# Optimization experiments

Hardware: AMD Instinct MI355X
Metric: run time of the kernel (lower is better)

Reference implementation:

```python
import jax, jax.numpy as jnp
import numpy as np

B, S = 64, 256
F, H, V = 512, 2048, 32000
PAD = 0
LN_EPS = 1e-5


def setup_inputs() -> dict:
    key = jax.random.key(0)
    ks = jax.random.split(key, 10)
    inputs = jax.random.randint(ks[0], (B, S), 0, V, dtype=jnp.int64)
    targets = jax.random.randint(ks[1], (B, S), 0, V, dtype=jnp.int64)
    # parameters (kaiming-ish / torch-default-ish scales)
    see = jax.random.normal(ks[2], (2 * F, F), jnp.float32) * (2.0 / (2 * F)) ** 0.5
    bias = jnp.zeros((F,), jnp.float32)
    W_in = jax.random.normal(ks[3], (H, F), jnp.float32) * (1.0 / F) ** 0.5
    b_in = jnp.zeros((H,), jnp.float32)
    W_out = jax.random.normal(ks[4], (F, H), jnp.float32) * (1.0 / H) ** 0.5
    b_out = jnp.zeros((F,), jnp.float32)
    ln_g = jnp.ones((F,), jnp.float32)
    ln_b = jnp.zeros((F,), jnp.float32)
    emb = jax.random.normal(ks[5], (V, F), jnp.float32)
    return {"inputs": inputs, "targets": targets, "see": see, "bias": bias,
            "W_in": W_in, "b_in": b_in, "W_out": W_out, "b_out": b_out,
            "ln_g": ln_g, "ln_b": ln_b, "emb": emb}


def _layernorm(x, g, b):
    mu = jnp.mean(x, axis=-1, keepdims=True)
    var = jnp.mean((x - mu) ** 2, axis=-1, keepdims=True)
    return (x - mu) * jax.lax.rsqrt(var + LN_EPS) * g + b


def reference(inputs, targets, see, bias, W_in, b_in, W_out, b_out, ln_g, ln_b, emb):
    emb_m = emb.at[PAD].set(0.0)  # padding_idx row is zero
    inv_sqrt_f = 1.0 / (F ** 0.5)

    def step(state, xy):
        idx, tgt = xy                      # [B], [B]
        vecs = emb_m[idx]                  # [B,F]
        gate = jax.nn.sigmoid(jnp.concatenate([vecs, state], axis=-1) @ see + bias)
        cont = state * gate + vecs * (1.0 - gate)
        h = jax.nn.relu(_layernorm(cont, ln_g, ln_b) @ W_in.T + b_in)
        out = h @ W_out.T + b_out          # [B,F]
        logits = (out @ emb_m.T) * inv_sqrt_f  # [B,V]
        logp = jax.nn.log_softmax(logits, axis=-1)
        nll = -jnp.take_along_axis(logp, tgt[:, None], axis=1)[:, 0]
        mask = (tgt != PAD).astype(logits.dtype)
        li = jnp.sum(nll * mask) / jnp.maximum(jnp.sum(mask), 1.0)
        return cont, li

    xs = (inputs.T, targets.T)  # [S,B]
    _, losses = jax.lax.scan(step, jnp.zeros((inputs.shape[0], F), emb.dtype), xs)
    return jnp.mean(losses)
```

## Files before the change

### kernel.cpp

```cpp
#include <hip/hip_runtime.h>
#include <hip/hip_fp8.h>

#define F_DIM 512
#define H_DIM 2048
#define V_DIM 32000
#define B_DIM 64
#define S_DIM 256
#define ROWS (S_DIM*B_DIM)
#define NT_LOG 250
#define SCALE 0.04419417382415922f
#define LSE_OFF 40.0f

typedef __attribute__((ext_vector_type(8))) short  short8;
typedef __attribute__((ext_vector_type(4))) float  floatx4;

static __device__ inline unsigned short f2bf(float x){
  unsigned int u = __float_as_uint(x);
  u += 0x7fffu + ((u >> 16) & 1u);
  return (unsigned short)(u >> 16);
}
static __device__ inline float bf2f(unsigned short u){
  return __uint_as_float(((unsigned int)u) << 16);
}
static __device__ inline unsigned char f2fp8(float x){
  __hip_fp8_e4m3 q(x);
  return q.__x;
}
static __device__ inline int sw8(int row, int col){
  int g = (col >> 3) & 7;
  int chunk = ((g >> 1) ^ ((row >> 1) & 3));
  int lob = (g & 1) ^ ((row >> 3) & 1);
  return (col & ~63) | (chunk << 4) | (lob << 3) | (col & 7);
}
static __device__ inline float wsum(float v){
  #pragma unroll
  for(int m = 32; m > 0; m >>= 1) v += __shfl_xor(v, m);
  return v;
}
static __device__ inline void load_lds16(const void* g, void* l){
  __builtin_amdgcn_global_load_lds((const __attribute__((address_space(1))) void*)g,
                                   (__attribute__((address_space(3))) void*)l, 16, 0, 0);
}

__global__ __launch_bounds__(256) void cast_w(const float* __restrict__ src,
                                              unsigned short* __restrict__ dst, int n){
  int i = blockIdx.x*256 + threadIdx.x;
  int stride = gridDim.x*256;
  for(; i < n; i += stride) dst[i] = f2bf(src[i]);
}
__global__ __launch_bounds__(256) void cast_emb(const float* __restrict__ src,
    unsigned short* __restrict__ dst, unsigned char* __restrict__ d8){
  int i = blockIdx.x*256 + threadIdx.x;
  int stride = gridDim.x*256;
  for(; i < V_DIM*F_DIM; i += stride){
    float v = (i < F_DIM) ? 0.f : src[i];
    dst[i] = f2bf(v);
    int row = i >> 9, col = i & 511;
    d8[(long)row*512 + sw8(row, col)] = f2fp8(v);
  }
}

__global__ __launch_bounds__(256) void prep_see(const float* __restrict__ see,
    unsigned short* __restrict__ TT, unsigned char* __restrict__ B8){
  int n = blockIdx.x;
  for(int k = threadIdx.x; k < 512; k += 256){
    TT[n*512 + k] = f2bf(see[(long)k*512 + n]);
    B8[n*512 + k] = f2fp8(see[(long)(512+k)*512 + n]);
  }
}

__global__ __launch_bounds__(256) void gather_vecs(const float* __restrict__ emb,
    const int* __restrict__ inp, unsigned short* __restrict__ V){
  long row = (long)blockIdx.x*4 + (threadIdx.x >> 6);
  int l = threadIdx.x & 63;
  int t = (int)(row >> 6), b = (int)(row & 63);
  int idx = inp[b*S_DIM + t];
  short8 o;
  if (idx == 0){
    #pragma unroll
    for(int i=0;i<8;i++) o[i] = 0;
  } else {
    const float* e = emb + (long)idx*F_DIM + l*8;
    float4 a = *(const float4*)e;
    float4 bq = *(const float4*)(e + 4);
    o[0]=(short)f2bf(a.x); o[1]=(short)f2bf(a.y); o[2]=(short)f2bf(a.z); o[3]=(short)f2bf(a.w);
    o[4]=(short)f2bf(bq.x);o[5]=(short)f2bf(bq.y);o[6]=(short)f2bf(bq.z);o[7]=(short)f2bf(bq.w);
  }
  *(short8*)(V + row*F_DIM + l*8) = o;
}

__global__ __launch_bounds__(512, 1) void recurrence_batch(
    const unsigned int* __restrict__ ZV,
    const unsigned char* __restrict__ W8,
    unsigned short* __restrict__ CONTB)
{
  __shared__ unsigned char stt[2][16][520];

  const int tid = threadIdx.x;
  const int w  = tid >> 6;
  const int l  = tid & 63;
  const int rl = l & 15, rq = l >> 4;
  const int wg = blockIdx.x;
  const int colb = w*64;

  long Bfr[16][4];
  #pragma unroll
  for(int c=0;c<16;c++)
    #pragma unroll
    for(int tl=0;tl<4;tl++)
      Bfr[c][tl] = *(const long*)(W8 + (long)(colb + tl*16 + rl)*512 + c*32 + rq*8);

  float s_old[16];
  #pragma unroll
  for(int i=0;i<16;i++) s_old[i] = 0.f;

  const unsigned int* zbase = ZV + (long)(wg*16 + rq*4)*512 + colb + rl;
  unsigned short* cbase = CONTB + ((long)wg*16 + rq*4)*512 + colb + rl;

  unsigned int zv[16];
  #pragma unroll
  for(int tl=0;tl<4;tl++)
    #pragma unroll
    for(int r=0;r<4;r++)
      zv[tl*4+r] = zbase[(long)r*512 + tl*16];

  for(int t = 0; t < S_DIM; t++){
    unsigned int zvn[16];
    if (t+1 < S_DIM){
      const unsigned int* zp = zbase + (long)(t+1)*64*512;
      #pragma unroll
      for(int tl=0;tl<4;tl++)
        #pragma unroll
        for(int r=0;r<4;r++)
          zvn[tl*4+r] = zp[(long)r*512 + tl*16];
    }

    asm volatile("s_waitcnt lgkmcnt(0)" ::: "memory");
    __builtin_amdgcn_s_barrier();
    asm volatile("" ::: "memory");

    floatx4 acc[4];
    #pragma unroll
    for(int tl=0;tl<4;tl++) acc[tl] = (floatx4)0.f;

    if (t > 0){
      const unsigned char* sb = &stt[(t-1)&1][0][0];
      #pragma unroll
      for(int c=0;c<16;c++){
        long a = *(const long*)(sb + rl*520 + c*32 + rq*8);
        #pragma unroll
        for(int tl=0;tl<4;tl++)
          acc[tl] = __builtin_amdgcn_mfma_f32_16x16x32_fp8_fp8(a, Bfr[c][tl], acc[tl], 0, 0, 0);
      }
    }

    unsigned short* cw = cbase + (long)t*64*512;
    unsigned char* swb = &stt[t&1][0][0] + rq*4*520 + colb + rl;
    #pragma unroll
    for(int tl=0;tl<4;tl++){
      float sv[4];
      #pragma unroll
      for(int r=0;r<4;r++){
        unsigned int p = zv[tl*4+r];
        float z = __uint_as_float(p << 16) + acc[tl][r];
        float v = __uint_as_float(p & 0xffff0000u);
        float e = __expf(-z);
        float g = __builtin_amdgcn_rcpf(1.f + e);
        float s = fmaf(s_old[tl*4+r] - v, g, v);
        s_old[tl*4+r] = s;
        sv[r] = s;
      }
      #pragma unroll
      for(int pr=0; pr<2; pr++){
        unsigned int bfp, f8p;
        asm("v_cvt_pk_bf16_f32 %0, %1, %2" : "=v"(bfp) : "v"(sv[pr*2]), "v"(sv[pr*2+1]));
        asm("v_cvt_pk_fp8_f32 %0, %1, %2"  : "=v"(f8p) : "v"(sv[pr*2]), "v"(sv[pr*2+1]));
        cw[(long)(pr*2)*512   + tl*16] = (unsigned short)(bfp & 0xffffu);
        cw[(long)(pr*2+1)*512 + tl*16] = (unsigned short)(bfp >> 16);
        swb[(pr*2)*520   + tl*16] = (unsigned char)(f8p & 0xffu);
        swb[(pr*2+1)*520 + tl*16] = (unsigned char)((f8p >> 8) & 0xffu);
      }
    }

    if (t+1 < S_DIM){
      #pragma unroll
      for(int i=0;i<16;i++) zv[i] = zvn[i];
    }
  }
}

__global__ __launch_bounds__(256) void ln_kernel(const unsigned short* __restrict__ contb,
    const float* __restrict__ lg, const float* __restrict__ lb,
    unsigned short* __restrict__ xln)
{
  const int wid = threadIdx.x >> 6, l = threadIdx.x & 63;
  const long row = (long)blockIdx.x*4 + wid;
  short8 xv = *(const short8*)(contb + row*F_DIM + l*8);
  float v[8];
  #pragma unroll
  for(int i=0;i<8;i++) v[i] = bf2f((unsigned short)xv[i]);
  float s = 0.f;
  #pragma unroll
  for(int i=0;i<8;i++) s += v[i];
  s = wsum(s);
  float mu = s * (1.f/512.f);
  float q = 0.f;
  #pragma unroll
  for(int i=0;i<8;i++){ float d = v[i]-mu; q += d*d; }
  q = wsum(q);
  float rs = rsqrtf(q*(1.f/512.f) + 1e-5f);
  short8 o;
  #pragma unroll
  for(int i=0;i<8;i++)
    o[i] = (short)f2bf((v[i]-mu)*rs*lg[l*8+i] + lb[l*8+i]);
  *(short8*)(xln + row*F_DIM + l*8) = o;
}

template<int MODE>
__global__ __launch_bounds__(256) void gemm_bt(
    const unsigned short* __restrict__ A,
    const unsigned short* __restrict__ Bm,
    const float* __restrict__ bias,
    unsigned short* __restrict__ C,
    unsigned char* __restrict__ C8,
    const unsigned short* __restrict__ Vsrc,
    unsigned int* __restrict__ ZVout,
    int M, int N, int K, int tiles_m, int tiles_n)
{
  __shared__ short As[128*64];
  __shared__ short Bs[128*64];

  const int bid = blockIdx.x;
  const int mt = bid % tiles_m;
  const int nt = bid / tiles_m;
  const long m0 = (long)mt * 128;
  const long n0 = (long)nt * 128;
  const int tid = threadIdx.x;
  const int l = tid & 63;
  const int wid = tid >> 6;
  const int wr = wid >> 1, wc = wid & 1;
  const int rl = l & 15, rq = l >> 4;

  const short* Ag = (const short*)A + m0 * K;
  const short* Bg = (const short*)Bm + n0 * K;
  const int grow = tid >> 3;
  const int kp = tid & 7;
  const int ksw = (kp ^ (grow & 7)) * 8;

  floatx4 acc[4][4];
  #pragma unroll
  for(int i=0;i<4;i++)
    #pragma unroll
    for(int j=0;j<4;j++) acc[i][j] = (floatx4)0.f;

  for(int k0 = 0; k0 < K; k0 += 64){
    __syncthreads();
    #pragma unroll
    for(int ro = 0; ro < 128; ro += 32){
      load_lds16(Ag + (long)(ro + grow)*K + k0 + ksw, (void*)(As + (ro+grow)*64 + kp*8));
      load_lds16(Bg + (long)(ro + grow)*K + k0 + ksw, (void*)(Bs + (ro+grow)*64 + kp*8));
    }
    __syncthreads();
    #pragma unroll
    for(int kb = 0; kb < 64; kb += 32){
      const int cb = kb >> 3;
      const int cl = ((cb + rq) ^ (rl & 7)) * 8;
      short8 af[4], bfr[4];
      #pragma unroll
      for(int i=0;i<4;i++) af[i]  = *(const short8*)(As + (wr*64 + i*16 + rl)*64 + cl);
      #pragma unroll
      for(int j=0;j<4;j++) bfr[j] = *(const short8*)(Bs + (wc*64 + j*16 + rl)*64 + cl);
      #pragma unroll
      for(int i=0;i<4;i++)
        #pragma unroll
        for(int j=0;j<4;j++)
          acc[i][j] = __builtin_amdgcn_mfma_f32_16x16x32_bf16(af[i], bfr[j], acc[i][j], 0, 0, 0);
    }
  }

  const long mb = m0 + wr*64;
  const long nb = n0 + wc*64;
  #pragma unroll
  for(int j=0;j<4;j++){
    float bj = bias[nb + j*16 + rl];
    #pragma unroll
    for(int i=0;i<4;i++){
      #pragma unroll
      for(int r=0;r<4;r++){
        float v = acc[i][j][r] + bj;
        if (MODE == 0) v = fmaxf(v, 0.f);
        int rowI = (int)(mb + i*16 + rq*4 + r);
        int colI = (int)(nb + j*16 + rl);
        long idx = (long)rowI*N + colI;
        if (MODE == 5){
          ZVout[idx] = ((unsigned)Vsrc[idx] << 16) | (unsigned)f2bf(v);
        } else {
          C[idx] = f2bf(v);
          if (MODE == 4) C8[(long)rowI*512 + sw8(rowI, colI)] = f2fp8(v);
        }
      }
    }
  }
}

__global__ __launch_bounds__(256) void gemm_f8_logits(
    const unsigned char* __restrict__ A8,
    const unsigned char* __restrict__ B8,
    float* __restrict__ part,
    int M, int N, int K, int tiles_m, int tiles_n)
{
  __shared__ unsigned char As8[2][128*64];
  __shared__ unsigned char Bs8[2][128*64];
  __shared__ float sm2[2][64][2];

  const int bid = blockIdx.x;
  const int mt = bid % tiles_m;
  const int nt = bid / tiles_m;
  const long m0 = (long)mt * 128;
  const long n0 = (long)nt * 128;
  const int tid = threadIdx.x;
  const int l = tid & 63;
  const int wid = tid >> 6;
  const int wr = wid >> 1, wc = wid & 1;
  const int rl = l & 15, rq = l >> 4;

  const unsigned char* Ag = A8 + m0 * K;
  const unsigned char* Bg = B8 + n0 * K;
  const int grow = tid >> 2;
  const int kp = tid & 3;

  floatx4 acc[4][4];
  #pragma unroll
  for(int i=0;i<4;i++)
    #pragma unroll
    for(int j=0;j<4;j++) acc[i][j] = (floatx4)0.f;

  const int rsw = (rl >> 1) & 3;
  const int rhi = (rl >> 3) & 1;

  const int nkt = K >> 6;

  #define STAGE_F8(bb, kk) do {                                               \
    const long kof = (long)(kk)*64 + kp*16;                                   \
    load_lds16(Ag + (long)grow*K       + kof, (void*)(&As8[bb][grow*64       + kp*16])); \
    load_lds16(Ag + (long)(64+grow)*K  + kof, (void*)(&As8[bb][(64+grow)*64  + kp*16])); \
    load_lds16(Bg + (long)grow*K       + kof, (void*)(&Bs8[bb][grow*64       + kp*16])); \
    load_lds16(Bg + (long)(64+grow)*K  + kof, (void*)(&Bs8[bb][(64+grow)*64  + kp*16])); \
  } while(0)

  STAGE_F8(0, 0);
  STAGE_F8(1, 1);

  for(int t = 0; t < nkt; t++){
    if (t < nkt-1) asm volatile("s_waitcnt vmcnt(4)" ::: "memory");
    else           asm volatile("s_waitcnt vmcnt(0)" ::: "memory");
    __builtin_amdgcn_s_barrier();
    __builtin_amdgcn_sched_barrier(0);

    const unsigned char* Abuf = &As8[t & 1][0];
    const unsigned char* Bbuf = &Bs8[t & 1][0];
    long af[2][4], bfr[2][4];
    #pragma unroll
    for(int kb = 0; kb < 2; kb++){
      const int g = (kb << 2) + rq;
      const int cl = ((((g >> 1) ^ rsw)) << 4) | ((((g & 1) ^ rhi)) << 3);
      #pragma unroll
      for(int i=0;i<4;i++) af[kb][i]  = *(const long*)(Abuf + (wr*64 + i*16 + rl)*64 + cl);
      #pragma unroll
      for(int j=0;j<4;j++) bfr[kb][j] = *(const long*)(Bbuf + (wc*64 + j*16 + rl)*64 + cl);
    }
    asm volatile("s_waitcnt lgkmcnt(0)" ::: "memory");
    __builtin_amdgcn_sched_barrier(0);
    __builtin_amdgcn_s_barrier();
    __builtin_amdgcn_sched_barrier(0);

    if (t+2 < nkt) STAGE_F8(t & 1, t+2);

    __builtin_amdgcn_s_setprio(1);
    #pragma unroll
    for(int kb = 0; kb < 2; kb++)
      #pragma unroll
      for(int i=0;i<4;i++)
        #pragma unroll
        for(int j=0;j<4;j++)
          acc[i][j] = __builtin_amdgcn_mfma_f32_16x16x32_fp8_fp8(af[kb][i], bfr[kb][j], acc[i][j], 0, 0, 0);
    __builtin_amdgcn_s_setprio(0);
  }
  #undef STAGE_F8

  #pragma unroll
  for(int i=0;i<4;i++){
    #pragma unroll
    for(int r=0;r<4;r++){
      float sv = 0.f;
      #pragma unroll
      for(int j=0;j<4;j++) sv += __expf(acc[i][j][r]*SCALE - LSE_OFF);
      #pragma unroll
      for(int d=1; d<16; d<<=1) sv += __shfl_xor(sv, d);
      if (rl == 0) sm2[wr][i*16 + rq*4 + r][wc] = sv;
    }
  }
  __syncthreads();
  if (tid < 128){
    int wr2 = tid >> 6, rowl = tid & 63;
    part[(m0 + wr2*64 + rowl)*tiles_n + nt] = sm2[wr2][rowl][0] + sm2[wr2][rowl][1];
  }
}

__global__ __launch_bounds__(256) void tlogit_kernel(const unsigned short* __restrict__ outb,
    const unsigned short* __restrict__ embb, const int* __restrict__ tgt,
    float* __restrict__ TL)
{
  long gw = (long)blockIdx.x*4 + (threadIdx.x >> 6);
  int l = threadIdx.x & 63;
  int t = (int)(gw >> 6), b = (int)(gw & 63);
  int tg = tgt[b*S_DIM + t];
  const unsigned short* o = outb + gw*F_DIM;
  const unsigned short* e = embb + (long)tg*F_DIM;
  short8 ov = *(const short8*)(o + l*8);
  short8 ev = *(const short8*)(e + l*8);
  float s = 0.f;
  #pragma unroll
  for(int i=0;i<8;i++) s += bf2f((unsigned short)ov[i]) * bf2f((unsigned short)ev[i]);
  s = wsum(s);
  if (l == 0) TL[gw] = s * SCALE;
}

__global__ __launch_bounds__(256) void lse_kernel(const float* __restrict__ part,
    const float* __restrict__ TL, float* __restrict__ nll)
{
  long row = (long)blockIdx.x*4 + (threadIdx.x >> 6);
  int l = threadIdx.x & 63;
  float S = 0.f;
  for(int c = l; c < NT_LOG; c += 64)
    S += part[row*NT_LOG + c];
  S = wsum(S);
  if (l == 0) nll[row] = (LSE_OFF + logf(S)) - TL[row];
}

__global__ __launch_bounds__(256) void loss_kernel(const float* __restrict__ nll,
    const int* __restrict__ tgt, float* __restrict__ out)
{
  int t = threadIdx.x;
  float s = 0.f; int cnt = 0;
  for(int b = 0; b < B_DIM; b++){
    int v = tgt[b*S_DIM + t];
    if (v != 0){ s += nll[(long)t*B_DIM + b]; cnt++; }
  }
  float li = s / fmaxf((float)cnt, 1.f);
  li = wsum(li);
  __shared__ float red[4];
  if ((t & 63) == 0) red[t >> 6] = li;
  __syncthreads();
  if (t == 0) out[0] = (red[0]+red[1]+red[2]+red[3]) * (1.f/256.f);
}

extern "C" void kernel_launch(void* const* d_in, const int* in_sizes, int n_in,
                              void* d_out, int out_size, void* d_ws, size_t ws_size,
                              hipStream_t stream)
{
  const int*   inp   = (const int*)d_in[0];
  const int*   tgt   = (const int*)d_in[1];
  const float* see   = (const float*)d_in[2];
  const float* bias  = (const float*)d_in[3];
  const float* W_in  = (const float*)d_in[4];
  const float* b_in  = (const float*)d_in[5];
  const float* W_out = (const float*)d_in[6];
  const float* b_out = (const float*)d_in[7];
  const float* ln_g  = (const float*)d_in[8];
  const float* ln_b  = (const float*)d_in[9];
  const float* emb   = (const float*)d_in[10];

  char* p = (char*)d_ws;
  unsigned short* CONTB= (unsigned short*)p; p += (size_t)ROWS*F_DIM*2;
  unsigned short* Hb   = (unsigned short*)p; p += (size_t)ROWS*H_DIM*2;
  unsigned short* OUTb = (unsigned short*)p; p += (size_t)ROWS*F_DIM*2;
  unsigned short* EMBb = (unsigned short*)p; p += (size_t)V_DIM*F_DIM*2;
  unsigned char* EMB8  = (unsigned char*)p;  p += (size_t)V_DIM*F_DIM;
  unsigned short* WINb = (unsigned short*)p; p += (size_t)H_DIM*F_DIM*2;
  unsigned short* WOUTb= (unsigned short*)p; p += (size_t)F_DIM*H_DIM*2;
  float* TL            = (float*)p;          p += (size_t)ROWS*4;
  float* NLL           = (float*)p;          p += (size_t)ROWS*4;
  unsigned short* VECSb= (unsigned short*)p; p += (size_t)ROWS*F_DIM*2;
  unsigned int* ZV     = (unsigned int*)p;   p += (size_t)ROWS*F_DIM*4;
  unsigned short* SEETT= (unsigned short*)p; p += (size_t)F_DIM*F_DIM*2;
  unsigned char* SEEB8 = (unsigned char*)p;  p += (size_t)F_DIM*F_DIM;
  unsigned short* XLN  = (unsigned short*)ZV;
  unsigned char* OUT8  = (unsigned char*)VECSb;
  float* PART          = (float*)Hb;

  cast_emb<<<4096, 256, 0, stream>>>(emb, EMBb, EMB8);
  cast_w<<<2048, 256, 0, stream>>>(W_in,  WINb,  H_DIM*F_DIM);
  cast_w<<<2048, 256, 0, stream>>>(W_out, WOUTb, F_DIM*H_DIM);
  prep_see<<<512, 256, 0, stream>>>(see, SEETT, SEEB8);
  gather_vecs<<<ROWS/4, 256, 0, stream>>>(emb, inp, VECSb);

  gemm_bt<5><<<128*4, 256, 0, stream>>>(VECSb, SEETT, bias, nullptr, nullptr,
                                        VECSb, ZV, ROWS, F_DIM, F_DIM, 128, 4);

  recurrence_batch<<<4, 512, 0, stream>>>(ZV, SEEB8, CONTB);

  ln_kernel<<<ROWS/4, 256, 0, stream>>>(CONTB, ln_g, ln_b, XLN);
  gemm_bt<0><<<128*16, 256, 0, stream>>>(XLN,  WINb,  b_in,  Hb,   nullptr,
                                         nullptr, nullptr, ROWS, H_DIM, F_DIM, 128, 16);
  gemm_bt<4><<<128*4,  256, 0, stream>>>(Hb,   WOUTb, b_out, OUTb, OUT8,
                                         nullptr, nullptr, ROWS, F_DIM, H_DIM, 128, 4);
  tlogit_kernel<<<ROWS/4, 256, 0, stream>>>(OUTb, EMBb, tgt, TL);
  gemm_f8_logits<<<128*NT_LOG, 256, 0, stream>>>(OUT8, EMB8, PART, ROWS, V_DIM, F_DIM, 128, NT_LOG);
  lse_kernel<<<ROWS/4, 256, 0, stream>>>(PART, TL, NLL);
  loss_kernel<<<1, 256, 0, stream>>>(NLL, tgt, (float*)d_out);
}
```

Baseline: 1.269 ms.

## Use 16x16x128 scaled FP8 MFMA and vectorized permuted ZV loads in recurrence

The serial recurrence kernel replaces 16 K-steps of 16x16x32 fp8 MFMA with 4 K-steps of the gfx950 16x16x128 scaled f8f6f4 MFMA, using unit scales. The A fragments now come from LDS as 32-byte reads, with the row pitch padded from 520 to 560. The ZV producer GEMM writes columns in a permuted order so each thread can read its 16 z/v values as four 128-bit loads. The next-step ZV prefetch moves to the end of the loop. The goal is fewer MFMA issues and fewer load instructions on the latency-bound sequential critical path. The risk is that the later prefetch exposes global-load latency.

```diff
diff --git a/kernel.cpp b/kernel.cpp
--- a/kernel.cpp
+++ b/kernel.cpp
@@ -13,6 +13,9 @@
 
 typedef __attribute__((ext_vector_type(8))) short  short8;
 typedef __attribute__((ext_vector_type(4))) float  floatx4;
+typedef __attribute__((ext_vector_type(4))) int    intx4;
+typedef __attribute__((ext_vector_type(8))) int    i32x8;
+typedef __attribute__((ext_vector_type(4))) unsigned int uix4;
 
 static __device__ inline unsigned short f2bf(float x){
   unsigned int u = __float_as_uint(x);
@@ -31,6 +34,9 @@
   int chunk = ((g >> 1) ^ ((row >> 1) & 3));
   int lob = (g & 1) ^ ((row >> 3) & 1);
   return (col & ~63) | (chunk << 4) | (lob << 3) | (col & 7);
+}
+static __device__ inline int zvperm(int c){
+  return (c & ~63) | ((c & 15) << 2) | ((c >> 4) & 3);
 }
 static __device__ inline float wsum(float v){
   #pragma unroll
@@ -94,7 +100,7 @@
     const unsigned char* __restrict__ W8,
     unsigned short* __restrict__ CONTB)
 {
-  __shared__ unsigned char stt[2][16][520];
+  __shared__ unsigned char stt[2][16][560];
 
   const int tid = threadIdx.x;
   const int w  = tid >> 6;
@@ -103,38 +109,25 @@
   const int wg = blockIdx.x;
   const int colb = w*64;
 
-  long Bfr[16][4];
-  #pragma unroll
-  for(int c=0;c<16;c++)
+  i32x8 Bfr[4][4];
+  #pragma unroll
+  for(int kt=0;kt<4;kt++)
     #pragma unroll
     for(int tl=0;tl<4;tl++)
-      Bfr[c][tl] = *(const long*)(W8 + (long)(colb + tl*16 + rl)*512 + c*32 + rq*8);
+      Bfr[kt][tl] = *(const i32x8*)(W8 + (long)(colb + tl*16 + rl)*512 + kt*128 + rq*32);
 
   float s_old[16];
   #pragma unroll
   for(int i=0;i<16;i++) s_old[i] = 0.f;
 
-  const unsigned int* zbase = ZV + (long)(wg*16 + rq*4)*512 + colb + rl;
+  const unsigned int* zbase = ZV + (long)(wg*16 + rq*4)*512 + colb + rl*4;
   unsigned short* cbase = CONTB + ((long)wg*16 + rq*4)*512 + colb + rl;
 
-  unsigned int zv[16];
-  #pragma unroll
-  for(int tl=0;tl<4;tl++)
-    #pragma unroll
-    for(int r=0;r<4;r++)
-      zv[tl*4+r] = zbase[(long)r*512 + tl*16];
+  uix4 zv[4];
+  #pragma unroll
+  for(int r=0;r<4;r++) zv[r] = *(const uix4*)(zbase + (long)r*512);
 
   for(int t = 0; t < S_DIM; t++){
-    unsigned int zvn[16];
-    if (t+1 < S_DIM){
-      const unsigned int* zp = zbase + (long)(t+1)*64*512;
-      #pragma unroll
-      for(int tl=0;tl<4;tl++)
-        #pragma unroll
-        for(int r=0;r<4;r++)
-          zvn[tl*4+r] = zp[(long)r*512 + tl*16];
-    }
-
     asm volatile("s_waitcnt lgkmcnt(0)" ::: "memory");
     __builtin_amdgcn_s_barrier();
     asm volatile("" ::: "memory");
@@ -143,25 +136,35 @@
     #pragma unroll
     for(int tl=0;tl<4;tl++) acc[tl] = (floatx4)0.f;
 
+    i32x8 afr[4];
     if (t > 0){
-      const unsigned char* sb = &stt[(t-1)&1][0][0];
-      #pragma unroll
-      for(int c=0;c<16;c++){
-        long a = *(const long*)(sb + rl*520 + c*32 + rq*8);
+      const unsigned char* sb = &stt[(t-1)&1][0][0] + rl*560 + rq*32;
+      #pragma unroll
+      for(int kt=0;kt<4;kt++){
+        intx4 a0 = *(const intx4*)(sb + kt*128);
+        intx4 a1 = *(const intx4*)(sb + kt*128 + 16);
+        afr[kt] = __builtin_shufflevector(a0, a1, 0,1,2,3,4,5,6,7);
+      }
+    }
+
+    unsigned short* cw = cbase + (long)t*64*512;
+    unsigned char* swb = &stt[t&1][0][0] + rq*4*560 + colb + rl;
+
+    #pragma unroll
+    for(int tl=0;tl<4;tl++){
+      if (t > 0){
         #pragma unroll
-        for(int tl=0;tl<4;tl++)
-          acc[tl] = __builtin_amdgcn_mfma_f32_16x16x32_fp8_fp8(a, Bfr[c][tl], acc[tl], 0, 0, 0);
+        for(int kt=0;kt<4;kt++)
+          acc[tl] = __builtin_amdgcn_mfma_scale_f32_16x16x128_f8f6f4(
+                        afr[kt], Bfr[kt][tl], acc[tl],
+                        0, 0,
+                        0, 0x7f7f7f7f,
+                        0, 0x7f7f7f7f);
       }
-    }
-
-    unsigned short* cw = cbase + (long)t*64*512;
-    unsigned char* swb = &stt[t&1][0][0] + rq*4*520 + colb + rl;
-    #pragma unroll
-    for(int tl=0;tl<4;tl++){
       float sv[4];
       #pragma unroll
       for(int r=0;r<4;r++){
-        unsigned int p = zv[tl*4+r];
+        unsigned int p = zv[r][tl];
         float z = __uint_as_float(p << 16) + acc[tl][r];
         float v = __uint_as_float(p & 0xffff0000u);
         float e = __expf(-z);
@@ -177,14 +180,15 @@
         asm("v_cvt_pk_fp8_f32 %0, %1, %2"  : "=v"(f8p) : "v"(sv[pr*2]), "v"(sv[pr*2+1]));
         cw[(long)(pr*2)*512   + tl*16] = (unsigned short)(bfp & 0xffffu);
         cw[(long)(pr*2+1)*512 + tl*16] = (unsigned short)(bfp >> 16);
-        swb[(pr*2)*520   + tl*16] = (unsigned char)(f8p & 0xffu);
-        swb[(pr*2+1)*520 + tl*16] = (unsigned char)((f8p >> 8) & 0xffu);
+        swb[(pr*2)*560   + tl*16] = (unsigned char)(f8p & 0xffu);
+        swb[(pr*2+1)*560 + tl*16] = (unsigned char)((f8p >> 8) & 0xffu);
       }
     }
 
     if (t+1 < S_DIM){
-      #pragma unroll
-      for(int i=0;i<16;i++) zv[i] = zvn[i];
+      const unsigned int* zp = zbase + (long)(t+1)*64*512;
+      #pragma unroll
+      for(int r=0;r<4;r++) zv[r] = *(const uix4*)(zp + (long)r*512);
     }
   }
 }
@@ -293,7 +297,8 @@
         int colI = (int)(nb + j*16 + rl);
         long idx = (long)rowI*N + colI;
         if (MODE == 5){
-          ZVout[idx] = ((unsigned)Vsrc[idx] << 16) | (unsigned)f2bf(v);
+          ZVout[(long)rowI*N + zvperm(colI)] =
+              ((unsigned)Vsrc[idx] << 16) | (unsigned)f2bf(v);
         } else {
           C[idx] = f2bf(v);
           if (MODE == 4) C8[(long)rowI*512 + sw8(rowI, colI)] = f2fp8(v);
```

Measured after the change: 1.151 ms. 1.1x faster.
